# Performance work log

Hardware: AMD Instinct MI355X
Metric: run time of the kernel (lower is better)

The kernel has to match this reference:

```python
import jax, jax.numpy as jnp
import numpy as np

COMMITMENT_COST = 0.25


def setup_inputs() -> dict:
    key = jax.random.key(0)
    k1, k2 = jax.random.split(key)
    B, T, D = 32, 256, 512
    K = 8192
    x = jax.random.normal(k1, (B, T, D), dtype=jnp.float32)
    # nn.Embedding init: uniform(-1/K, 1/K)
    embeddings = jax.random.uniform(k2, (K, D), dtype=jnp.float32,
                                    minval=-1.0 / K, maxval=1.0 / K)
    return {"x": x, "embeddings": embeddings}


def reference(x, embeddings):
    orig_shape = x.shape
    D = orig_shape[-1]
    x_flat = x.reshape(-1, D)                      # [N, D]

    # squared Euclidean distances via expansion (argmin-equivalent to cdist)
    x_sq = jnp.sum(x_flat * x_flat, axis=1, keepdims=True)     # [N, 1]
    e_sq = jnp.sum(embeddings * embeddings, axis=1)            # [K]
    dots = jnp.einsum('nd,kd->nk', x_flat, embeddings)         # [N, K]
    distances = x_sq - 2.0 * dots + e_sq[None, :]              # [N, K]

    indices = jnp.argmin(distances, axis=1)                    # [N]
    quantized = embeddings[indices].reshape(orig_shape)        # [..., D]
    indices = indices.reshape(orig_shape[:-1])

    commitment_loss = jnp.mean((x - jax.lax.stop_gradient(quantized)) ** 2) * COMMITMENT_COST
    codebook_loss = jnp.mean((quantized - jax.lax.stop_gradient(x)) ** 2)
    total_loss = commitment_loss + codebook_loss

    # straight-through estimator
    quantized_st = x + jax.lax.stop_gradient(quantized - x)
    return quantized_st, indices, commitment_loss, codebook_loss, total_loss
```

## Files before the change

kernel.cpp:

```cpp
#include <hip/hip_runtime.h>

#define N_ROWS 8192
#define K_CODES 8192
#define D_DIM 512

typedef unsigned long long u64;

__global__ __launch_bounds__(256) void vq_sq(const float* __restrict__ x,
                                             const float* __restrict__ emb,
                                             float* __restrict__ x_sq,
                                             float* __restrict__ e_sq) {
  const int t = threadIdx.x;
  const int wave = t >> 6, l = t & 63;
  const int half = l >> 5, ll = l & 31;
  const int q = ll >> 3, j = ll & 7;
  const int row = blockIdx.x * 8 + wave * 2 + half;
  const float* p =
      (row < N_ROWS) ? (x + (size_t)row * D_DIM)
                     : (emb + (size_t)(row - N_ROWS) * D_DIM);
  const float v0 = p[128 * q + j];
  float r = __fmul_rn(v0, v0);
#pragma unroll
  for (int i = 1; i < 16; ++i) {
    const float v = p[128 * q + 8 * i + j];
    r = __fadd_rn(r, __fmul_rn(v, v));
  }
  r = __fadd_rn(r, __shfl_xor(r, 1, 64));
  r = __fadd_rn(r, __shfl_xor(r, 2, 64));
  r = __fadd_rn(r, __shfl_xor(r, 4, 64));
  r = __fadd_rn(r, __shfl_xor(r, 8, 64));
  r = __fadd_rn(r, __shfl_xor(r, 16, 64));
  if (ll == 0) {
    if (row < N_ROWS) x_sq[row] = r;
    else e_sq[row - N_ROWS] = r;
  }
}

__device__ __forceinline__ void compute_chunk(const float* __restrict__ esb,
                                              const float* __restrict__ xw,
                                              int dd0, int lane,
                                              float (&acc)[8][2]) {
  const int rbase = lane * 64;
  const int lm = lane & 7;
#pragma unroll
  for (int g = 0; g < 8; ++g) {
    const float* p = esb + rbase + 4 * (g ^ lm);
    const float4 ev0 = *reinterpret_cast<const float4*>(p);
    const float4 ev1 = *reinterpret_cast<const float4*>(p + 32);
#pragma unroll
    for (int r = 0; r < 8; ++r) {
      const float4 xv =
          *reinterpret_cast<const float4*>(xw + r * D_DIM + dd0 + 4 * g);
      float a0 = acc[r][0], a1 = acc[r][1];
      a0 = __fmaf_rn(xv.x, ev0.x, a0);
      a0 = __fmaf_rn(xv.y, ev0.y, a0);
      a0 = __fmaf_rn(xv.z, ev0.z, a0);
      a0 = __fmaf_rn(xv.w, ev0.w, a0);
      a1 = __fmaf_rn(xv.x, ev1.x, a1);
      a1 = __fmaf_rn(xv.y, ev1.y, a1);
      a1 = __fmaf_rn(xv.z, ev1.z, a1);
      a1 = __fmaf_rn(xv.w, ev1.w, a1);
      acc[r][0] = a0;
      acc[r][1] = a1;
    }
  }
}

#define STAGE(BUF, ESRC)                                                       \
  do {                                                                         \
    __builtin_amdgcn_global_load_lds(                                          \
        (const __attribute__((address_space(1))) void*)(ESRC),                 \
        (__attribute__((address_space(3))) void*)(&es[BUF][4 * t]), 16, 0, 0); \
    __builtin_amdgcn_global_load_lds(                                          \
        (const __attribute__((address_space(1))) void*)((ESRC) + 32 * D_DIM), \
        (__attribute__((address_space(3))) void*)(&es[BUF][4 * t + 1024]),     \
        16, 0, 0);                                                             \
    __builtin_amdgcn_global_load_lds(                                          \
        (const __attribute__((address_space(1))) void*)((ESRC) + 64 * D_DIM), \
        (__attribute__((address_space(3))) void*)(&es[BUF][4 * t + 2048]),     \
        16, 0, 0);                                                             \
    __builtin_amdgcn_global_load_lds(                                          \
        (const __attribute__((address_space(1))) void*)((ESRC) + 96 * D_DIM), \
        (__attribute__((address_space(3))) void*)(&es[BUF][4 * t + 3072]),     \
        16, 0, 0);                                                             \
  } while (0)

__global__ __launch_bounds__(256, 4) void vq_dist(
    const float* __restrict__ x, const float* __restrict__ e,
    const float* __restrict__ x_sq, const float* __restrict__ e_sq,
    u64* __restrict__ slots) {
  __shared__ float es[2][4096];

  const int t = threadIdx.x;
  const int lane = t & 63;

  const int bx = blockIdx.x;
  const int swz = (bx & 7) * 2048 + (bx >> 3);
  const int kb = swz >> 8;
  const int nb = swz & 255;
  const int k0 = kb * 128;
  const int n0w = __builtin_amdgcn_readfirstlane(nb * 32 + (t >> 6) * 8);
  const float* xw = x + (size_t)n0w * D_DIM;

  const float* esrc =
      e + (size_t)(k0 + (t >> 3)) * D_DIM + 4 * ((t & 7) ^ ((t >> 4) & 7));

  float accA[8][2], accB[8][2];
#pragma unroll
  for (int r = 0; r < 8; ++r) {
    accA[r][0] = 0.0f; accA[r][1] = 0.0f;
    accB[r][0] = 0.0f; accB[r][1] = 0.0f;
  }

  STAGE(0, esrc);
  asm volatile("s_waitcnt vmcnt(0)" ::: "memory");
  __syncthreads();

#pragma unroll 1
  for (int c = 0; c < 12; ++c) {
    STAGE((c + 1) & 1, esrc + (c + 1) * 32);
    compute_chunk(&es[c & 1][0], xw, c * 32, lane, accA);
    asm volatile("s_waitcnt vmcnt(0)" ::: "memory");
    __syncthreads();
  }
#pragma unroll 1
  for (int c = 12; c < 16; ++c) {
    if (c < 15) STAGE((c + 1) & 1, esrc + (c + 1) * 32);
    compute_chunk(&es[c & 1][0], xw, c * 32, lane, accB);
    asm volatile("s_waitcnt vmcnt(0)" ::: "memory");
    __syncthreads();
  }

  const float4 xsqa = *reinterpret_cast<const float4*>(x_sq + n0w);
  const float4 xsqb = *reinterpret_cast<const float4*>(x_sq + n0w + 4);
  const float xsq[8] = {xsqa.x, xsqa.y, xsqa.z, xsqa.w,
                        xsqb.x, xsqb.y, xsqb.z, xsqb.w};
  const int klane = k0 + 2 * lane;
  const float2 esq = *reinterpret_cast<const float2*>(e_sq + klane);
  const float esqv[2] = {esq.x, esq.y};

#pragma unroll
  for (int r = 0; r < 8; ++r) {
    u64 best = ~0ULL;
#pragma unroll
    for (int j = 0; j < 2; ++j) {
      float dot = __fadd_rn(accA[r][j], accB[r][j]);
      float dist = __fadd_rn(__fsub_rn(xsq[r], __fmul_rn(2.0f, dot)), esqv[j]);
      unsigned int b = __float_as_uint(dist);
      unsigned int sb = (b & 0x80000000u) ? ~b : (b | 0x80000000u);
      u64 key = ((u64)sb << 32) | (unsigned)(klane + j);
      best = best < key ? best : key;
    }
#pragma unroll
    for (int off = 32; off > 0; off >>= 1) {
      u64 o = __shfl_xor((unsigned long long)best, off, 64);
      best = best < o ? best : o;
    }
    if (lane == 0) atomicMin(&slots[n0w + r], best);
  }
}

__global__ __launch_bounds__(256) void vq_out(
    const float* __restrict__ x, const float* __restrict__ e,
    const u64* __restrict__ slots, float* __restrict__ out_q,
    float* __restrict__ out_idx, double* __restrict__ loss_part) {
  const int t = threadIdx.x;
  const int w = t >> 6, lane = t & 63;
  const int n = blockIdx.x * 4 + w;
  const int idx = (int)(slots[n] & 0xFFFFFFFFULL);
  const float4* qr = (const float4*)(e + (size_t)idx * D_DIM);
  const float4* xr = (const float4*)(x + (size_t)n * D_DIM);
  float4* outr = (float4*)(out_q + (size_t)n * D_DIM);
  double s = 0.0;
#pragma unroll
  for (int i = 0; i < 2; ++i) {
    const int d4 = lane * 2 + i;
    float4 q = qr[d4];
    float4 xv = xr[d4];
    outr[d4] = q;
    double d0 = (double)xv.x - (double)q.x;
    double d1 = (double)xv.y - (double)q.y;
    double d2 = (double)xv.z - (double)q.z;
    double d3 = (double)xv.w - (double)q.w;
    s += d0 * d0 + d1 * d1 + d2 * d2 + d3 * d3;
  }
  for (int off = 32; off > 0; off >>= 1) s += __shfl_down(s, off, 64);
  if (lane == 0) {
    out_idx[n] = (float)idx;
    atomicAdd(&loss_part[(n * 37) & 255], s);
  }
}

__global__ void vq_loss(const double* __restrict__ loss_part,
                        float* __restrict__ out_s) {
  __shared__ double sm[256];
  const int t = threadIdx.x;
  sm[t] = loss_part[t];
  __syncthreads();
  for (int off = 128; off > 0; off >>= 1) {
    if (t < off) sm[t] += sm[t + off];
    __syncthreads();
  }
  if (t == 0) {
    double m = sm[0] / (double)(N_ROWS * D_DIM);
    out_s[0] = (float)(0.25 * m);
    out_s[1] = (float)m;
    out_s[2] = (float)(1.25 * m);
  }
}

extern "C" void kernel_launch(void* const* d_in, const int* in_sizes, int n_in,
                              void* d_out, int out_size, void* d_ws, size_t ws_size,
                              hipStream_t stream) {
  const float* x = (const float*)d_in[0];
  const float* emb = (const float*)d_in[1];
  float* out = (float*)d_out;

  u64* slots = (u64*)d_ws;
  float* x_sq = (float*)((char*)d_ws + 65536);
  float* e_sq = (float*)((char*)d_ws + 98304);
  double* loss_part = (double*)((char*)d_ws + 131072);

  hipMemsetAsync(d_ws, 0xFF, 65536, stream);
  hipMemsetAsync(loss_part, 0, 256 * sizeof(double), stream);

  vq_sq<<<2048, 256, 0, stream>>>(x, emb, x_sq, e_sq);
  vq_dist<<<16384, 256, 0, stream>>>(x, emb, x_sq, e_sq, slots);
  vq_out<<<N_ROWS / 4, 256, 0, stream>>>(x, emb, slots, out,
                                         out + N_ROWS * D_DIM, loss_part);
  vq_loss<<<1, 256, 0, stream>>>(loss_part, out + N_ROWS * D_DIM + N_ROWS);
}
```

Baseline: 936.7 us.

## Widen distance tile to 256 codes per block with 4 codes per lane

Each vq_dist block now covers 256 codebook entries instead of 128, and each lane accumulates 4 codes per row instead of 2. The D-chunk per stage shrinks from 32 to 16 floats so the LDS buffer stays the same size. The aim is to reuse each x float4 load across twice as many FMAs and to halve the number of blocks, cutting x reloads and atomicMin traffic. The cost is more accumulator registers, a drop in the launch-bound occupancy target from 4 to 2 blocks, and twice as many sync-separated stages.

```diff
diff --git a/kernel.cpp b/kernel.cpp
--- a/kernel.cpp
+++ b/kernel.cpp
@@ -36,22 +36,24 @@
   }
 }
 
-__device__ __forceinline__ void compute_chunk(const float* __restrict__ esb,
-                                              const float* __restrict__ xw,
-                                              int dd0, int lane,
-                                              float (&acc)[8][2]) {
+__device__ __forceinline__ void compute_chunk16(const float* __restrict__ esb,
+                                                const float* __restrict__ xw,
+                                                int dd0, int lane,
+                                                float (&acc)[8][4]) {
   const int rbase = lane * 64;
-  const int lm = lane & 7;
-#pragma unroll
-  for (int g = 0; g < 8; ++g) {
+  const int lm = lane & 3;
+#pragma unroll
+  for (int g = 0; g < 4; ++g) {
     const float* p = esb + rbase + 4 * (g ^ lm);
     const float4 ev0 = *reinterpret_cast<const float4*>(p);
-    const float4 ev1 = *reinterpret_cast<const float4*>(p + 32);
+    const float4 ev1 = *reinterpret_cast<const float4*>(p + 16);
+    const float4 ev2 = *reinterpret_cast<const float4*>(p + 32);
+    const float4 ev3 = *reinterpret_cast<const float4*>(p + 48);
 #pragma unroll
     for (int r = 0; r < 8; ++r) {
       const float4 xv =
           *reinterpret_cast<const float4*>(xw + r * D_DIM + dd0 + 4 * g);
-      float a0 = acc[r][0], a1 = acc[r][1];
+      float a0 = acc[r][0], a1 = acc[r][1], a2 = acc[r][2], a3 = acc[r][3];
       a0 = __fmaf_rn(xv.x, ev0.x, a0);
       a0 = __fmaf_rn(xv.y, ev0.y, a0);
       a0 = __fmaf_rn(xv.z, ev0.z, a0);
@@ -60,8 +62,15 @@
       a1 = __fmaf_rn(xv.y, ev1.y, a1);
       a1 = __fmaf_rn(xv.z, ev1.z, a1);
       a1 = __fmaf_rn(xv.w, ev1.w, a1);
-      acc[r][0] = a0;
-      acc[r][1] = a1;
+      a2 = __fmaf_rn(xv.x, ev2.x, a2);
+      a2 = __fmaf_rn(xv.y, ev2.y, a2);
+      a2 = __fmaf_rn(xv.z, ev2.z, a2);
+      a2 = __fmaf_rn(xv.w, ev2.w, a2);
+      a3 = __fmaf_rn(xv.x, ev3.x, a3);
+      a3 = __fmaf_rn(xv.y, ev3.y, a3);
+      a3 = __fmaf_rn(xv.z, ev3.z, a3);
+      a3 = __fmaf_rn(xv.w, ev3.w, a3);
+      acc[r][0] = a0; acc[r][1] = a1; acc[r][2] = a2; acc[r][3] = a3;
     }
   }
 }
@@ -72,20 +81,20 @@
         (const __attribute__((address_space(1))) void*)(ESRC),                 \
         (__attribute__((address_space(3))) void*)(&es[BUF][4 * t]), 16, 0, 0); \
     __builtin_amdgcn_global_load_lds(                                          \
-        (const __attribute__((address_space(1))) void*)((ESRC) + 32 * D_DIM), \
+        (const __attribute__((address_space(1))) void*)((ESRC) + 64 * D_DIM),  \
         (__attribute__((address_space(3))) void*)(&es[BUF][4 * t + 1024]),     \
         16, 0, 0);                                                             \
     __builtin_amdgcn_global_load_lds(                                          \
-        (const __attribute__((address_space(1))) void*)((ESRC) + 64 * D_DIM), \
+        (const __attribute__((address_space(1))) void*)((ESRC) + 128 * D_DIM), \
         (__attribute__((address_space(3))) void*)(&es[BUF][4 * t + 2048]),     \
         16, 0, 0);                                                             \
     __builtin_amdgcn_global_load_lds(                                          \
-        (const __attribute__((address_space(1))) void*)((ESRC) + 96 * D_DIM), \
+        (const __attribute__((address_space(1))) void*)((ESRC) + 192 * D_DIM), \
         (__attribute__((address_space(3))) void*)(&es[BUF][4 * t + 3072]),     \
         16, 0, 0);                                                             \
   } while (0)
 
-__global__ __launch_bounds__(256, 4) void vq_dist(
+__global__ __launch_bounds__(256, 2) void vq_dist(
     const float* __restrict__ x, const float* __restrict__ e,
     const float* __restrict__ x_sq, const float* __restrict__ e_sq,
     u64* __restrict__ slots) {
@@ -93,40 +102,40 @@
 
   const int t = threadIdx.x;
   const int lane = t & 63;
+  const int w = t >> 6;
 
   const int bx = blockIdx.x;
-  const int swz = (bx & 7) * 2048 + (bx >> 3);
+  const int swz = (bx & 7) * 1024 + (bx >> 3);
   const int kb = swz >> 8;
   const int nb = swz & 255;
-  const int k0 = kb * 128;
-  const int n0w = __builtin_amdgcn_readfirstlane(nb * 32 + (t >> 6) * 8);
+  const int k0 = kb * 256;
+  const int n0w = __builtin_amdgcn_readfirstlane(nb * 32 + w * 8);
   const float* xw = x + (size_t)n0w * D_DIM;
 
   const float* esrc =
-      e + (size_t)(k0 + (t >> 3)) * D_DIM + 4 * ((t & 7) ^ ((t >> 4) & 7));
-
-  float accA[8][2], accB[8][2];
-#pragma unroll
-  for (int r = 0; r < 8; ++r) {
-    accA[r][0] = 0.0f; accA[r][1] = 0.0f;
-    accB[r][0] = 0.0f; accB[r][1] = 0.0f;
-  }
+      e + (size_t)(k0 + (t >> 2)) * D_DIM + 4 * ((t & 3) ^ ((t >> 4) & 3));
+
+  float accA[8][4], accB[8][4];
+#pragma unroll
+  for (int r = 0; r < 8; ++r)
+#pragma unroll
+    for (int j = 0; j < 4; ++j) { accA[r][j] = 0.0f; accB[r][j] = 0.0f; }
 
   STAGE(0, esrc);
   asm volatile("s_waitcnt vmcnt(0)" ::: "memory");
   __syncthreads();
 
 #pragma unroll 1
-  for (int c = 0; c < 12; ++c) {
-    STAGE((c + 1) & 1, esrc + (c + 1) * 32);
-    compute_chunk(&es[c & 1][0], xw, c * 32, lane, accA);
+  for (int c = 0; c < 24; ++c) {
+    STAGE((c + 1) & 1, esrc + (c + 1) * 16);
+    compute_chunk16(&es[c & 1][0], xw, c * 16, lane, accA);
     asm volatile("s_waitcnt vmcnt(0)" ::: "memory");
     __syncthreads();
   }
 #pragma unroll 1
-  for (int c = 12; c < 16; ++c) {
-    if (c < 15) STAGE((c + 1) & 1, esrc + (c + 1) * 32);
-    compute_chunk(&es[c & 1][0], xw, c * 32, lane, accB);
+  for (int c = 24; c < 32; ++c) {
+    if (c < 31) STAGE((c + 1) & 1, esrc + (c + 1) * 16);
+    compute_chunk16(&es[c & 1][0], xw, c * 16, lane, accB);
     asm volatile("s_waitcnt vmcnt(0)" ::: "memory");
     __syncthreads();
   }
@@ -135,15 +144,15 @@
   const float4 xsqb = *reinterpret_cast<const float4*>(x_sq + n0w + 4);
   const float xsq[8] = {xsqa.x, xsqa.y, xsqa.z, xsqa.w,
                         xsqb.x, xsqb.y, xsqb.z, xsqb.w};
-  const int klane = k0 + 2 * lane;
-  const float2 esq = *reinterpret_cast<const float2*>(e_sq + klane);
-  const float esqv[2] = {esq.x, esq.y};
+  const int klane = k0 + 4 * lane;
+  const float4 esq = *reinterpret_cast<const float4*>(e_sq + klane);
+  const float esqv[4] = {esq.x, esq.y, esq.z, esq.w};
 
 #pragma unroll
   for (int r = 0; r < 8; ++r) {
     u64 best = ~0ULL;
 #pragma unroll
-    for (int j = 0; j < 2; ++j) {
+    for (int j = 0; j < 4; ++j) {
       float dot = __fadd_rn(accA[r][j], accB[r][j]);
       float dist = __fadd_rn(__fsub_rn(xsq[r], __fmul_rn(2.0f, dot)), esqv[j]);
       unsigned int b = __float_as_uint(dist);
@@ -225,7 +234,7 @@
   hipMemsetAsync(loss_part, 0, 256 * sizeof(double), stream);
 
   vq_sq<<<2048, 256, 0, stream>>>(x, emb, x_sq, e_sq);
-  vq_dist<<<16384, 256, 0, stream>>>(x, emb, x_sq, e_sq, slots);
+  vq_dist<<<8192, 256, 0, stream>>>(x, emb, x_sq, e_sq, slots);
   vq_out<<<N_ROWS / 4, 256, 0, stream>>>(x, emb, slots, out,
                                          out + N_ROWS * D_DIM, loss_part);
   vq_loss<<<1, 256, 0, stream>>>(loss_part, out + N_ROWS * D_DIM + N_ROWS);
```

Result: faster. 901.9 us (-3.7%).
